# Kernel tuning notes

Measured on AMD Instinct MI355X. Metric: run time of the kernel, lower is better.

The kernel has to match this reference:

```python
import jax, jax.numpy as jnp
import numpy as np

EPS = 1e-12  # matches torch F.normalize default eps
WEIGHT = jnp.array([1.0, 1.0, 1.0], dtype=jnp.float32)  # per-channel loss weights


def _l2norm(x, axis):
    # torch F.normalize: x / max(||x||_2, eps)
    n = jnp.sqrt(jnp.sum(x * x, axis=axis, keepdims=True))
    return x / jnp.maximum(n, EPS)


def setup_inputs() -> dict:
    key = jax.random.key(0)
    k1, k2 = jax.random.split(key)
    shape = (16, 3, 512, 512)  # [B, C, H, W]
    return {
        "x": jax.random.normal(k1, shape, dtype=jnp.float32),
        "ref": jax.random.normal(k2, shape, dtype=jnp.float32),
    }


def reference(x, ref):
    # trace(rownorm(A) @ rownorm(B)^T) == sum(rownorm(A) * rownorm(B));
    # trace(colnorm(A)^T @ colnorm(B)) == sum(colnorm(A) * colnorm(B)).
    B, C, H, W = x.shape
    # per (batch, channel) traces, vectorized over all dims
    a = jnp.sum(_l2norm(x, -1) * _l2norm(ref, -1), axis=(-2, -1)) / H  # [B, C]
    b = jnp.sum(_l2norm(x, -2) * _l2norm(ref, -2), axis=(-2, -1)) / W  # [B, C]
    a = -jnp.sum(a * WEIGHT) / B
    b = -jnp.sum(b * WEIGHT) / B
    return a + b
```

## Files before the change

### kernel.cpp

```cpp
#include <hip/hip_runtime.h>

#define B_N 16
#define C_N 3
#define H_N 512
#define W_N 512
#define PLANES (B_N * C_N)
#define ROWS_PER_BLOCK 16
#define ROWS_PER_WAVE 4
#define CHUNKS (H_N / ROWS_PER_BLOCK)
#define NBLK (PLANES * CHUNKS)
#define STATS3 (W_N * 3)
#define SCALE (-1.0f / 8192.0f)
#define EPS_F 1e-12f

__global__ __launch_bounds__(256, 4) void spl_main_kernel(
    const float* __restrict__ x, const float* __restrict__ r,
    float* __restrict__ colpart, float* __restrict__ rowpart) {
    const int p     = blockIdx.x / CHUNKS;
    const int chunk = blockIdx.x % CHUNKS;
    const int wave  = threadIdx.x >> 6;
    const int lane  = threadIdx.x & 63;

    const float* xp = x + (size_t)p * (H_N * W_N);
    const float* rp = r + (size_t)p * (H_N * W_N);

    float cxx[8] = {0, 0, 0, 0, 0, 0, 0, 0};
    float crr[8] = {0, 0, 0, 0, 0, 0, 0, 0};
    float cxr[8] = {0, 0, 0, 0, 0, 0, 0, 0};
    float psxx[ROWS_PER_WAVE], psrr[ROWS_PER_WAVE], psxr[ROWS_PER_WAVE];

    const int r0 = chunk * ROWS_PER_BLOCK + wave * ROWS_PER_WAVE;
    #pragma unroll
    for (int j = 0; j < ROWS_PER_WAVE; ++j) {
        const int row = r0 + j;
        const float4* xr4 = (const float4*)(xp + (size_t)row * W_N);
        const float4* rr4 = (const float4*)(rp + (size_t)row * W_N);
        const float4 xa = xr4[lane];
        const float4 xb = xr4[lane + 64];
        const float4 ra = rr4[lane];
        const float4 rb = rr4[lane + 64];

        const float ax[8] = {xa.x, xa.y, xa.z, xa.w, xb.x, xb.y, xb.z, xb.w};
        const float rx[8] = {ra.x, ra.y, ra.z, ra.w, rb.x, rb.y, rb.z, rb.w};

        float sxx = 0.0f, srr = 0.0f, sxr = 0.0f;
        #pragma unroll
        for (int k = 0; k < 8; ++k) {
            const float txx = ax[k] * ax[k];
            const float trr = rx[k] * rx[k];
            const float txr = ax[k] * rx[k];
            cxx[k] += txx; crr[k] += trr; cxr[k] += txr;
            sxx += txx;    srr += trr;    sxr += txr;
        }
        psxx[j] = sxx; psrr[j] = srr; psxr[j] = sxr;
    }

    #pragma unroll
    for (int m = 32; m > 0; m >>= 1) {
        #pragma unroll
        for (int j = 0; j < ROWS_PER_WAVE; ++j) {
            psxx[j] += __shfl_down(psxx[j], m, 64);
            psrr[j] += __shfl_down(psrr[j], m, 64);
            psxr[j] += __shfl_down(psxr[j], m, 64);
        }
    }
    float rowacc = 0.0f;
    if (lane == 0) {
        #pragma unroll
        for (int j = 0; j < ROWS_PER_WAVE; ++j) {
            const float nx = fmaxf(sqrtf(psxx[j]), EPS_F);
            const float nr = fmaxf(sqrtf(psrr[j]), EPS_F);
            rowacc += psxr[j] / (nx * nr);
        }
    }

    __shared__ float smem[4][STATS3];
    #pragma unroll
    for (int k = 0; k < 4; ++k) {
        const int c0 = 4 * lane + k;
        const int c1 = c0 + 256;
        smem[wave][c0 * 3 + 0] = cxx[k];
        smem[wave][c0 * 3 + 1] = crr[k];
        smem[wave][c0 * 3 + 2] = cxr[k];
        smem[wave][c1 * 3 + 0] = cxx[4 + k];
        smem[wave][c1 * 3 + 1] = crr[4 + k];
        smem[wave][c1 * 3 + 2] = cxr[4 + k];
    }
    __shared__ float rowsums[4];
    if (lane == 0) rowsums[wave] = rowacc;
    __syncthreads();

    float* cp = colpart + (size_t)blockIdx.x * STATS3;
    #pragma unroll
    for (int k = 0; k < 6; ++k) {
        const int e = threadIdx.x + 256 * k;
        cp[e] = smem[0][e] + smem[1][e] + smem[2][e] + smem[3][e];
    }
    if (threadIdx.x == 0)
        rowpart[blockIdx.x] = rowsums[0] + rowsums[1] + rowsums[2] + rowsums[3];
}

__global__ __launch_bounds__(256) void spl_reduce_kernel(
    const float* __restrict__ colpart, const float* __restrict__ rowpart,
    float* __restrict__ planesum) {
    const int p = blockIdx.x;
    float acc[6] = {0, 0, 0, 0, 0, 0};
    const float* base = colpart + (size_t)p * CHUNKS * STATS3;
    for (int c = 0; c < CHUNKS; ++c) {
        const float* bc = base + c * STATS3;
        #pragma unroll
        for (int k = 0; k < 6; ++k) acc[k] += bc[threadIdx.x + 256 * k];
    }
    __shared__ float sums[STATS3];
    #pragma unroll
    for (int k = 0; k < 6; ++k) sums[threadIdx.x + 256 * k] = acc[k];
    __syncthreads();

    float term = 0.0f;
    #pragma unroll
    for (int k = 0; k < 2; ++k) {
        const int col = threadIdx.x + 256 * k;
        const float sxx = sums[col * 3 + 0];
        const float srr = sums[col * 3 + 1];
        const float sxr = sums[col * 3 + 2];
        term += sxr / (fmaxf(sqrtf(sxx), EPS_F) * fmaxf(sqrtf(srr), EPS_F));
    }
    if (threadIdx.x < CHUNKS) term += rowpart[p * CHUNKS + threadIdx.x];

    #pragma unroll
    for (int m = 32; m > 0; m >>= 1) term += __shfl_down(term, m, 64);
    __shared__ float ws[4];
    if ((threadIdx.x & 63) == 0) ws[threadIdx.x >> 6] = term;
    __syncthreads();
    if (threadIdx.x == 0) planesum[p] = ws[0] + ws[1] + ws[2] + ws[3];
}

__global__ void spl_final_kernel(const float* __restrict__ planesum,
                                 float* __restrict__ out) {
    float v = (threadIdx.x < PLANES) ? planesum[threadIdx.x] : 0.0f;
    #pragma unroll
    for (int m = 32; m > 0; m >>= 1) v += __shfl_down(v, m, 64);
    if (threadIdx.x == 0) out[0] = SCALE * v;
}

extern "C" void kernel_launch(void* const* d_in, const int* in_sizes, int n_in,
                              void* d_out, int out_size, void* d_ws, size_t ws_size,
                              hipStream_t stream) {
    const float* x   = (const float*)d_in[0];
    const float* ref = (const float*)d_in[1];
    float* out = (float*)d_out;

    float* colpart  = (float*)d_ws;
    float* rowpart  = colpart + (size_t)NBLK * STATS3;
    float* planesum = rowpart + NBLK;

    spl_main_kernel<<<NBLK, 256, 0, stream>>>(x, ref, colpart, rowpart);
    spl_reduce_kernel<<<PLANES, 256, 0, stream>>>(colpart, rowpart, planesum);
    spl_final_kernel<<<1, 64, 0, stream>>>(planesum, out);
}
```

Baseline: 126.0 us.

## Double rows per block and store column stats in planar shared layout

Each block now processes 32 rows (8 per wave, interleaved in two 16-row groups), which halves the number of blocks and the volume of per-block column partials written to and re-read from global memory. The shared-memory column statistics switch from an interleaved [col*3+stat] layout to a planar [stat][col] layout so that each wave can write them with float4 stores, and the reduce kernel's indexing is updated to match. The cost is fewer blocks in flight (1536 vs 3072) and more registers for the extra per-row partial sums, which could reduce latency hiding.

```diff
diff --git a/kernel.cpp b/kernel.cpp
--- a/kernel.cpp
+++ b/kernel.cpp
@@ -5,8 +5,8 @@
 #define H_N 512
 #define W_N 512
 #define PLANES (B_N * C_N)
-#define ROWS_PER_BLOCK 16
-#define ROWS_PER_WAVE 4
+#define ROWS_PER_BLOCK 32
+#define ROWS_PER_WAVE 8
 #define CHUNKS (H_N / ROWS_PER_BLOCK)
 #define NBLK (PLANES * CHUNKS)
 #define STATS3 (W_N * 3)
@@ -29,30 +29,34 @@
     float cxr[8] = {0, 0, 0, 0, 0, 0, 0, 0};
     float psxx[ROWS_PER_WAVE], psrr[ROWS_PER_WAVE], psxr[ROWS_PER_WAVE];
 
-    const int r0 = chunk * ROWS_PER_BLOCK + wave * ROWS_PER_WAVE;
+    const int r0 = chunk * ROWS_PER_BLOCK;
     #pragma unroll
-    for (int j = 0; j < ROWS_PER_WAVE; ++j) {
-        const int row = r0 + j;
-        const float4* xr4 = (const float4*)(xp + (size_t)row * W_N);
-        const float4* rr4 = (const float4*)(rp + (size_t)row * W_N);
-        const float4 xa = xr4[lane];
-        const float4 xb = xr4[lane + 64];
-        const float4 ra = rr4[lane];
-        const float4 rb = rr4[lane + 64];
+    for (int b = 0; b < 2; ++b) {
+        #pragma unroll
+        for (int j = 0; j < 4; ++j) {
+            const int row = r0 + b * 16 + wave * 4 + j;
+            const int jj = b * 4 + j;
+            const float4* xr4 = (const float4*)(xp + (size_t)row * W_N);
+            const float4* rr4 = (const float4*)(rp + (size_t)row * W_N);
+            const float4 xa = xr4[lane];
+            const float4 xb = xr4[lane + 64];
+            const float4 ra = rr4[lane];
+            const float4 rb = rr4[lane + 64];
 
-        const float ax[8] = {xa.x, xa.y, xa.z, xa.w, xb.x, xb.y, xb.z, xb.w};
-        const float rx[8] = {ra.x, ra.y, ra.z, ra.w, rb.x, rb.y, rb.z, rb.w};
+            const float ax[8] = {xa.x, xa.y, xa.z, xa.w, xb.x, xb.y, xb.z, xb.w};
+            const float rx[8] = {ra.x, ra.y, ra.z, ra.w, rb.x, rb.y, rb.z, rb.w};
 
-        float sxx = 0.0f, srr = 0.0f, sxr = 0.0f;
-        #pragma unroll
-        for (int k = 0; k < 8; ++k) {
-            const float txx = ax[k] * ax[k];
-            const float trr = rx[k] * rx[k];
-            const float txr = ax[k] * rx[k];
-            cxx[k] += txx; crr[k] += trr; cxr[k] += txr;
-            sxx += txx;    srr += trr;    sxr += txr;
+            float sxx = 0.0f, srr = 0.0f, sxr = 0.0f;
+            #pragma unroll
+            for (int k = 0; k < 8; ++k) {
+                const float txx = ax[k] * ax[k];
+                const float trr = rx[k] * rx[k];
+                const float txr = ax[k] * rx[k];
+                cxx[k] += txx; crr[k] += trr; cxr[k] += txr;
+                sxx += txx;    srr += trr;    sxr += txr;
+            }
+            psxx[jj] = sxx; psrr[jj] = srr; psxr[jj] = sxr;
         }
-        psxx[j] = sxx; psrr[j] = srr; psxr[j] = sxr;
     }
 
     #pragma unroll
@@ -74,18 +78,13 @@
         }
     }
 
-    __shared__ float smem[4][STATS3];
-    #pragma unroll
-    for (int k = 0; k < 4; ++k) {
-        const int c0 = 4 * lane + k;
-        const int c1 = c0 + 256;
-        smem[wave][c0 * 3 + 0] = cxx[k];
-        smem[wave][c0 * 3 + 1] = crr[k];
-        smem[wave][c0 * 3 + 2] = cxr[k];
-        smem[wave][c1 * 3 + 0] = cxx[4 + k];
-        smem[wave][c1 * 3 + 1] = crr[4 + k];
-        smem[wave][c1 * 3 + 2] = cxr[4 + k];
-    }
+    __shared__ float smem[4][3][W_N];
+    *(float4*)&smem[wave][0][4 * lane]       = make_float4(cxx[0], cxx[1], cxx[2], cxx[3]);
+    *(float4*)&smem[wave][0][4 * lane + 256] = make_float4(cxx[4], cxx[5], cxx[6], cxx[7]);
+    *(float4*)&smem[wave][1][4 * lane]       = make_float4(crr[0], crr[1], crr[2], crr[3]);
+    *(float4*)&smem[wave][1][4 * lane + 256] = make_float4(crr[4], crr[5], crr[6], crr[7]);
+    *(float4*)&smem[wave][2][4 * lane]       = make_float4(cxr[0], cxr[1], cxr[2], cxr[3]);
+    *(float4*)&smem[wave][2][4 * lane + 256] = make_float4(cxr[4], cxr[5], cxr[6], cxr[7]);
     __shared__ float rowsums[4];
     if (lane == 0) rowsums[wave] = rowacc;
     __syncthreads();
@@ -94,7 +93,7 @@
     #pragma unroll
     for (int k = 0; k < 6; ++k) {
         const int e = threadIdx.x + 256 * k;
-        cp[e] = smem[0][e] + smem[1][e] + smem[2][e] + smem[3][e];
+        cp[e] = smem[0][0][e] + smem[1][0][e] + smem[2][0][e] + smem[3][0][e];
     }
     if (threadIdx.x == 0)
         rowpart[blockIdx.x] = rowsums[0] + rowsums[1] + rowsums[2] + rowsums[3];
@@ -120,9 +119,9 @@
     #pragma unroll
     for (int k = 0; k < 2; ++k) {
         const int col = threadIdx.x + 256 * k;
-        const float sxx = sums[col * 3 + 0];
-        const float srr = sums[col * 3 + 1];
-        const float sxr = sums[col * 3 + 2];
+        const float sxx = sums[col];
+        const float srr = sums[512 + col];
+        const float sxr = sums[1024 + col];
         term += sxr / (fmaxf(sqrtf(sxx), EPS_F) * fmaxf(sqrtf(srr), EPS_F));
     }
     if (threadIdx.x < CHUNKS) term += rowpart[p * CHUNKS + threadIdx.x];
```

After: 179.5 us. 42.4% more time.
